# Kernel tuning notes

Measured on AMD Instinct MI355X. Metric: run time of the kernel, lower is better.

## Reference

```python
import jax, jax.numpy as jnp
import numpy as np

SCORE_THR = 0.05
IOU_THR = 0.5
MAX_PER_IMG = 100
PRE_NMS_K = 2048  # fixed candidate budget for jit-compatible NMS
NUM_CLASSES = 80
MEANS = jnp.array([0.0, 0.0, 0.0, 0.0], jnp.float32)
STDS = jnp.array([0.1, 0.1, 0.2, 0.2], jnp.float32)
WH_RATIO_CLIP = 16.0 / 1000.0


def setup_inputs() -> dict:
    key = jax.random.key(0)
    B, N, C = 4, 8192, NUM_CLASSES
    H, W = 800, 1333
    k1, k2, k3, k4, k5, k6 = jax.random.split(key, 6)
    class_outs = jax.random.normal(k1, (B * N, C + 1), jnp.float32)
    regression_outs = jax.random.normal(k2, (B * N, C * 4), jnp.float32) * 0.5
    x1 = jax.random.uniform(k3, (B, N), minval=0.0, maxval=W * 0.8)
    y1 = jax.random.uniform(k4, (B, N), minval=0.0, maxval=H * 0.8)
    w = jax.random.uniform(k5, (B, N), minval=8.0, maxval=W * 0.2)
    h = jax.random.uniform(k6, (B, N), minval=8.0, maxval=H * 0.2)
    boxes = jnp.stack([x1, y1, jnp.minimum(x1 + w, float(W)), jnp.minimum(y1 + h, float(H))], axis=-1)
    return {"class_outs": class_outs, "regression_outs": regression_outs, "boxes": boxes, "img_h": H, "img_w": W}


def delta2bbox(proposals, deltas, H, W):
    # proposals [N,4], deltas [N, C*4] -> decoded boxes [N, C, 4]
    d = deltas.reshape(deltas.shape[0], -1, 4) * STDS + MEANS
    dx, dy, dw, dh = d[..., 0], d[..., 1], d[..., 2], d[..., 3]
    max_ratio = jnp.abs(jnp.log(jnp.float32(WH_RATIO_CLIP)))
    dw = jnp.clip(dw, -max_ratio, max_ratio)
    dh = jnp.clip(dh, -max_ratio, max_ratio)
    px = (proposals[:, 0] + proposals[:, 2]) * 0.5
    py = (proposals[:, 1] + proposals[:, 3]) * 0.5
    pw = proposals[:, 2] - proposals[:, 0]
    ph = proposals[:, 3] - proposals[:, 1]
    gx = px[:, None] + pw[:, None] * dx
    gy = py[:, None] + ph[:, None] * dy
    gw = pw[:, None] * jnp.exp(dw)
    gh = ph[:, None] * jnp.exp(dh)
    x1 = jnp.clip(gx - gw * 0.5, 0.0, float(W))
    y1 = jnp.clip(gy - gh * 0.5, 0.0, float(H))
    x2 = jnp.clip(gx + gw * 0.5, 0.0, float(W))
    y2 = jnp.clip(gy + gh * 0.5, 0.0, float(H))
    return jnp.stack([x1, y1, x2, y2], axis=-1)


def pairwise_iou(b):
    # b [K,4] -> [K,K]
    area = jnp.maximum(b[:, 2] - b[:, 0], 0.0) * jnp.maximum(b[:, 3] - b[:, 1], 0.0)
    lt = jnp.maximum(b[:, None, :2], b[None, :, :2])
    rb = jnp.minimum(b[:, None, 2:], b[None, :, 2:])
    wh = jnp.clip(rb - lt, 0.0)
    inter = wh[..., 0] * wh[..., 1]
    union = area[:, None] + area[None, :] - inter
    return inter / jnp.maximum(union, 1e-6)


def per_image(cls_out, reg_out, props, H, W):
    C = NUM_CLASSES
    scores = jax.nn.softmax(cls_out, axis=-1)[:, :C]        # drop background column
    bboxes = delta2bbox(props[:, :4], reg_out, H, W)        # [N, C, 4]
    flat_s = scores.reshape(-1)                             # [N*C]
    flat_s = jnp.where(flat_s > SCORE_THR, flat_s, -1.0)
    top_s, top_i = jax.lax.top_k(flat_s, PRE_NMS_K)
    cand = bboxes.reshape(-1, 4)[top_i]                     # [K,4]
    labels = top_i % C
    valid = top_s > 0.0
    # class-aware NMS via coordinate offsets per class
    offset = labels.astype(cand.dtype)[:, None] * (float(max(H, W)) + 1.0)
    iou = pairwise_iou(cand + offset)                       # [K,K]
    idx = jnp.arange(PRE_NMS_K)

    def body(i, keep):
        sup = (iou[i] > IOU_THR) & (idx > i) & keep[i]
        return keep & ~sup

    keep = jax.lax.fori_loop(0, PRE_NMS_K, body, valid)
    fs = jnp.where(keep, top_s, -1.0)
    out_s, order = jax.lax.top_k(fs, MAX_PER_IMG)
    ok = out_s > 0.0
    det_boxes = jnp.where(ok[:, None], cand[order], 0.0)
    det_scores = jnp.where(ok, out_s, 0.0)
    det_labels = jnp.where(ok, labels[order], -1)
    det_inds = jnp.where(ok, top_i[order], -1)
    return det_boxes, det_scores, det_labels, det_inds


def reference(class_outs, regression_outs, boxes, img_h, img_w):
    B, N = boxes.shape[:2]
    cls = class_outs.reshape(B, N, -1)
    reg = regression_outs.reshape(B, N, -1)
    f = jax.vmap(lambda c, r, p: per_image(c, r, p, img_h, img_w))
    det_boxes, det_scores, det_labels, det_inds = f(cls, reg, boxes)
    return det_boxes, det_scores, det_labels, det_inds
```

## Files before the change

### kernel.cpp

```cpp
#include <hip/hip_runtime.h>
#include <cstdint>
#include <cstddef>

#pragma clang fp contract(off)

typedef unsigned long long u64;
typedef unsigned int u32;

#define B_IMG 4
#define N_ROI 8192
#define NCLS 80
#define NCOL 81
#define K_NMS 2048
#define MAXOUT 100
#define THR_SCORE 0.05f
#define THR_IOU 0.5f

#define NBIN 4096
#define BIN_OFF 62771u
#define RPI 2048
#define BLKCAP 128
#define STGN 4096

__global__ __launch_bounds__(256) void k_score(const float* __restrict__ cls,
                                               u32* __restrict__ blkcnt,
                                               u64* __restrict__ glist) {
#pragma clang fp contract(off)
  int t = threadIdx.x, wv = t >> 6, lane = t & 63;
  int wreg = blockIdx.x * 4 + wv;
  int wid0 = wreg * 4;

  const float* row0 = cls + (size_t)(wid0 + 0) * NCOL;
  const float* row1 = cls + (size_t)(wid0 + 1) * NCOL;
  const float* row2 = cls + (size_t)(wid0 + 2) * NCOL;
  const float* row3 = cls + (size_t)(wid0 + 3) * NCOL;
  float a0 = row0[lane], a1 = row1[lane], a2 = row2[lane], a3 = row3[lane];
  bool hi = lane < (NCOL - 64);
  float b0 = hi ? row0[64 + lane] : -1e38f;
  float b1 = hi ? row1[64 + lane] : -1e38f;
  float b2 = hi ? row2[64 + lane] : -1e38f;
  float b3 = hi ? row3[64 + lane] : -1e38f;

  float m0 = fmaxf(a0, b0), m1 = fmaxf(a1, b1), m2 = fmaxf(a2, b2), m3 = fmaxf(a3, b3);
#define MAXSTEP(o) \
  m0 = fmaxf(m0, __shfl_xor(m0, o)); m1 = fmaxf(m1, __shfl_xor(m1, o)); \
  m2 = fmaxf(m2, __shfl_xor(m2, o)); m3 = fmaxf(m3, __shfl_xor(m3, o));
  MAXSTEP(32) MAXSTEP(16) MAXSTEP(8) MAXSTEP(4) MAXSTEP(2) MAXSTEP(1)
#undef MAXSTEP

  float e0 = expf(a0 - m0), e1 = expf(a1 - m1), e2 = expf(a2 - m2), e3 = expf(a3 - m3);
  float f0 = hi ? expf(b0 - m0) : 0.0f;
  float f1 = hi ? expf(b1 - m1) : 0.0f;
  float f2 = hi ? expf(b2 - m2) : 0.0f;
  float f3 = hi ? expf(b3 - m3) : 0.0f;
  float s0 = e0 + f0, s1 = e1 + f1, s2 = e2 + f2, s3 = e3 + f3;
#define SUMSTEP(o) \
  s0 += __shfl_xor(s0, o); s1 += __shfl_xor(s1, o); \
  s2 += __shfl_xor(s2, o); s3 += __shfl_xor(s3, o);
  SUMSTEP(32) SUMSTEP(16) SUMSTEP(8) SUMSTEP(4) SUMSTEP(2) SUMSTEP(1)
#undef SUMSTEP

  float p0 = e0 / s0, p1 = e1 / s1, p2 = e2 / s2, p3 = e3 / s3;
  float q0 = f0 / s0, q1 = f1 / s1, q2 = f2 / s2, q3 = f3 / s3;

  u64 lm = (1ull << lane) - 1ull;
  bool lo16 = lane < 16;
  u32 base = 0;
  u64* reg = glist + (size_t)wreg * BLKCAP;

#define EMIT(R, pv, qv)                                                    \
  {                                                                        \
    bool c0 = pv > THR_SCORE;                                              \
    bool c1 = lo16 && (qv > THR_SCORE);                                    \
    u64 B0 = __ballot(c0), B1 = __ballot(c1);                              \
    int n = (wid0 + R) & (N_ROI - 1);                                      \
    if (c0) {                                                              \
      u32 pos = base + (u32)__popcll(B0 & lm);                             \
      if (pos < BLKCAP) {                                                  \
        u32 flat = (u32)(n * NCLS + lane);                                 \
        reg[pos] = ((u64)__float_as_uint(pv) << 32) | (u32)(~flat);        \
      }                                                                    \
    }                                                                      \
    if (c1) {                                                              \
      u32 pos = base + (u32)__popcll(B0) + (u32)__popcll(B1 & lm);         \
      if (pos < BLKCAP) {                                                  \
        u32 flat = (u32)(n * NCLS + 64 + lane);                            \
        reg[pos] = ((u64)__float_as_uint(qv) << 32) | (u32)(~flat);        \
      }                                                                    \
    }                                                                      \
    base += (u32)(__popcll(B0) + __popcll(B1));                            \
  }

  EMIT(0, p0, q0)
  EMIT(1, p1, q1)
  EMIT(2, p2, q2)
  EMIT(3, p3, q3)
#undef EMIT

  if (lane == 0) blkcnt[wreg] = base;
}

__global__ __launch_bounds__(1024) void k_histcut(const u32* __restrict__ blkcnt,
                                                  const u64* __restrict__ glist,
                                                  u32* __restrict__ cutg,
                                                  u32* __restrict__ binbase,
                                                  u32* __restrict__ bincnt,
                                                  u32* __restrict__ keptT) {
  __shared__ u32 lh[NBIN];
  __shared__ u32 wsum[16];
  __shared__ int best;
  __shared__ u32 cutsh;
  int b = blockIdx.x, t = threadIdx.x;
  int lane = t & 63, wv = t >> 6;

  for (int i = t; i < NBIN; i += 1024) lh[i] = 0;
  __syncthreads();

  for (int r = t; r < RPI; r += 1024) {
    u32 cnt = blkcnt[b * RPI + r];
    if (cnt > BLKCAP) cnt = BLKCAP;
    const u64* reg = glist + ((size_t)(b * RPI + r)) * BLKCAP;
    for (u32 k = 0; k < cnt; ++k) {
      u64 key = reg[k];
      atomicAdd(&lh[(u32)(key >> 46) - BIN_OFF], 1u);
    }
  }
  if (t == 0) best = 0;
  __syncthreads();

  u32 v0 = lh[t * 4 + 0], v1 = lh[t * 4 + 1], v2 = lh[t * 4 + 2], v3 = lh[t * 4 + 3];
  u32 my = v0 + v1 + v2 + v3;
  u32 inc = my;
  for (int o = 1; o < 64; o <<= 1) {
    u32 x = __shfl_up(inc, o);
    if (lane >= o) inc += x;
  }
  if (lane == 63) wsum[wv] = inc;

  u32* bc = bincnt + (size_t)b * NBIN + t * 4;
  bc[0] = 0; bc[1] = 0; bc[2] = 0; bc[3] = 0;
  __syncthreads();

  u32 wpre = 0;
  for (int i = 0; i < wv; ++i) wpre += wsum[i];
  u32 total = 0;
  for (int i = 0; i < 16; ++i) total += wsum[i];
  u32 excl = wpre + (inc - my);

  u32* bb = binbase + (size_t)b * NBIN + t * 4;
  u32 pi = excl;
  pi += v0; bb[0] = total - pi;
  pi += v1; bb[1] = total - pi;
  pi += v2; bb[2] = total - pi;
  pi += v3; bb[3] = total - pi;

  if (total >= K_NMS) {
    u32 lim = total - K_NMS;
    u32 p = excl;
    int cand = -1;
    if (p <= lim) cand = t * 4 + 0; p += v0;
    if (p <= lim) cand = t * 4 + 1; p += v1;
    if (p <= lim) cand = t * 4 + 2; p += v2;
    if (p <= lim) cand = t * 4 + 3; p += v3;
    if (cand >= 0) atomicMax(&best, cand);
  }
  __syncthreads();
  if (t == 0) {
    u32 c = (total >= K_NMS) ? (u32)best : 0u;
    cutsh = c;
    cutg[b] = c;
  }
  __syncthreads();
  u32 c = cutsh;
  if (t == (int)(c >> 2)) {
    u32 pe = excl;
    int r = (int)(c & 3);
    if (r > 0) pe += v0;
    if (r > 1) pe += v1;
    if (r > 2) pe += v2;
    keptT[b] = total - pe;
  }
}

__global__ __launch_bounds__(256) void k_scatter(const u32* __restrict__ blkcnt,
                                                 const u64* __restrict__ glist,
                                                 const u32* __restrict__ cutg,
                                                 const u32* __restrict__ binbase,
                                                 u32* __restrict__ bincnt,
                                                 u64* __restrict__ staging) {
  __shared__ u32 lcnt[32];
  __shared__ u32 mshare;
  int blk = blockIdx.x;
  int b = blk >> 6;
  int r0 = (blk & 63) * 32;
  int t = threadIdx.x;
  if (t < 32) {
    u32 cc = blkcnt[b * RPI + r0 + t];
    lcnt[t] = (cc > BLKCAP) ? BLKCAP : cc;
  }
  __syncthreads();
  if (t == 0) {
    u32 m = 0;
    for (int i = 0; i < 32; ++i) m = (lcnt[i] > m) ? lcnt[i] : m;
    mshare = m;
  }
  __syncthreads();
  u32 mmax = mshare;
  u32 cut = cutg[b];
  int r = t >> 3;
  int k0 = t & 7;
  u32 cr = lcnt[r];
  const u64* regp = glist + ((size_t)(b * RPI + r0 + r)) * BLKCAP;
  for (u32 base = 0; base < mmax; base += 8) {
    u32 k = base + k0;
    if (k < cr) {
      u64 key = regp[k];
      u32 bin = (u32)(key >> 46) - BIN_OFF;
      if (bin >= cut) {
        u32 slot = binbase[(size_t)b * NBIN + bin] +
                   atomicAdd(&bincnt[(size_t)b * NBIN + bin], 1u);
        if (slot < STGN) staging[(size_t)b * STGN + slot] = key;
      }
    }
  }
}

__global__ __launch_bounds__(256) void k_rankdecode(const u32* __restrict__ keptT,
                                                    const u32* __restrict__ binbase,
                                                    const u32* __restrict__ bincnt,
                                                    const u64* __restrict__ staging,
                                                    const float* __restrict__ props,
                                                    const float* __restrict__ regs,
                                                    const int* __restrict__ pH,
                                                    const int* __restrict__ pW,
                                                    float4* __restrict__ raw4,
                                                    float4* __restrict__ off4,
                                                    float* __restrict__ area,
                                                    float* __restrict__ scoref,
                                                    int* __restrict__ labeli,
                                                    int* __restrict__ flati) {
#pragma clang fp contract(off)
  int p0 = blockIdx.x * 256 + threadIdx.x;
  int b = p0 >> 12;
  int i = p0 & (STGN - 1);
  u32 T = keptT[b];
  if (T > STGN) T = STGN;

  if ((u32)i >= T) {
    if ((u32)i < K_NMS) {
      size_t g = (size_t)b * K_NMS + i;
      raw4[g] = make_float4(0.f, 0.f, 0.f, 0.f);
      off4[g] = make_float4(0.f, 0.f, 0.f, 0.f);
      area[g] = 0.f; scoref[g] = -1.0f; labeli[g] = 0; flati[g] = 0;
    }
    return;
  }

  u64 key = staging[(size_t)b * STGN + i];
  u32 bin = (u32)(key >> 46) - BIN_OFF;
  u32 base = binbase[(size_t)b * NBIN + bin];
  u32 cnt = bincnt[(size_t)b * NBIN + bin];
  u32 end = base + cnt;
  if (end > STGN) end = STGN;
  u32 rank = 0;
  for (u32 j = base; j < end; ++j)
    rank += (staging[(size_t)b * STGN + j] > key) ? 1u : 0u;
  u32 gslot = base + rank;
  if (gslot >= K_NMS) return;
  size_t g = (size_t)b * K_NMS + gslot;

  float Hf = (float)pH[0];
  float Wf = (float)pW[0];
  float offc = fmaxf(Hf, Wf) + 1.0f;

  u32 flat = ~(u32)(key & 0xFFFFFFFFull);
  float sc = __uint_as_float((u32)(key >> 32));
  int n = (int)(flat / NCLS);
  int c = (int)(flat - (u32)n * NCLS);

  float4 p = ((const float4*)props)[b * N_ROI + n];
  const float4 dl = *(const float4*)(regs + ((size_t)(b * N_ROI + n)) * (NCLS * 4) + c * 4);

  float mr = fabsf(logf(16.0f / 1000.0f));
  float dx = dl.x * 0.1f;
  float dy = dl.y * 0.1f;
  float dw = fminf(fmaxf(dl.z * 0.2f, -mr), mr);
  float dh = fminf(fmaxf(dl.w * 0.2f, -mr), mr);

  float px = (p.x + p.z) * 0.5f;
  float py = (p.y + p.w) * 0.5f;
  float pw = p.z - p.x;
  float ph = p.w - p.y;

  float tx = pw * dx; float gx = px + tx;
  float ty = ph * dy; float gy = py + ty;
  float gw = pw * expf(dw);
  float gh = ph * expf(dh);
  float hx = gw * 0.5f, hy = gh * 0.5f;

  float x1 = fminf(fmaxf(gx - hx, 0.0f), Wf);
  float y1 = fminf(fmaxf(gy - hy, 0.0f), Hf);
  float x2 = fminf(fmaxf(gx + hx, 0.0f), Wf);
  float y2 = fminf(fmaxf(gy + hy, 0.0f), Hf);

  raw4[g] = make_float4(x1, y1, x2, y2);

  float off = (float)c * offc;
  float ox1 = x1 + off, oy1 = y1 + off, ox2 = x2 + off, oy2 = y2 + off;
  off4[g] = make_float4(ox1, oy1, ox2, oy2);
  area[g] = fmaxf(ox2 - ox1, 0.0f) * fmaxf(oy2 - oy1, 0.0f);
  scoref[g] = sc;
  labeli[g] = c;
  flati[g] = (int)flat;
}

__global__ __launch_bounds__(256) void k_mask(const float4* __restrict__ off4,
                                              const float* __restrict__ area,
                                              u64* __restrict__ masks) {
#pragma clang fp contract(off)
  int wave = threadIdx.x >> 6, lane = threadIdx.x & 63;
  int R = blockIdx.x * 4 + wave;
  int b = R >> 11, i = R & (K_NMS - 1);
  const float4* bb = off4 + (size_t)b * K_NMS;
  const float* aa = area + (size_t)b * K_NMS;
  float4 bi = bb[i];
  float ai = aa[i];
  u64 my = 0;
  for (int w = i >> 6; w < 32; ++w) {
    int j = (w << 6) + lane;
    float4 bj = bb[j];
    float lx = fmaxf(bi.x, bj.x);
    float ly = fmaxf(bi.y, bj.y);
    float rx = fminf(bi.z, bj.z);
    float ry = fminf(bi.w, bj.w);
    float ww = fmaxf(rx - lx, 0.0f);
    float hh = fmaxf(ry - ly, 0.0f);
    float inter = ww * hh;
    float uni = (ai + aa[j]) - inter;
    float iou = inter / fmaxf(uni, 1e-6f);
    bool sup = (j > i) && (iou > THR_IOU);
    u64 word = __ballot(sup);
    if (lane == w) my = word;
  }
  if (lane < 32) masks[((size_t)R << 5) + lane] = my;
}

__global__ __launch_bounds__(64, 1) void k_scanout(const u64* __restrict__ masks,
                                                   const u32* __restrict__ keptT,
                                                   const float* __restrict__ scoref,
                                                   const float4* __restrict__ raw4,
                                                   const int* __restrict__ labeli,
                                                   const int* __restrict__ flati,
                                                   float* __restrict__ out) {
  int b = blockIdx.x;
  int lane = threadIdx.x;

  u32 Tc = keptT[b];
  if (Tc > K_NMS) Tc = K_NMS;
  u64 kw = 0;
  if (lane < 32) {
    int rem = (int)Tc - (lane << 6);
    kw = (rem >= 64) ? ~0ull : ((rem > 0) ? ((1ull << rem) - 1ull) : 0ull);
  }

  const u64* mrow = masks + ((size_t)b << 16);
  int myw = lane & 31;
  int half = lane >> 5;

  u64 dnext = mrow[((size_t)lane << 5) + 0];

  for (int c = 0; c < 32; ++c) {
    u64 dcur = dnext;
    if (c < 31) dnext = mrow[((size_t)((c + 1) * 64 + lane) << 5) + (c + 1)];

    const u64* rb = mrow + (((size_t)(c * 64 + half * 32)) << 5) + myw;
    u64 r0 = rb[0u << 5],  r1 = rb[1u << 5],  r2 = rb[2u << 5],  r3 = rb[3u << 5];
    u64 r4 = rb[4u << 5],  r5 = rb[5u << 5],  r6 = rb[6u << 5],  r7 = rb[7u << 5];
    u64 r8 = rb[8u << 5],  r9 = rb[9u << 5],  r10 = rb[10u << 5], r11 = rb[11u << 5];
    u64 r12 = rb[12u << 5], r13 = rb[13u << 5], r14 = rb[14u << 5], r15 = rb[15u << 5];
    u64 r16 = rb[16u << 5], r17 = rb[17u << 5], r18 = rb[18u << 5], r19 = rb[19u << 5];
    u64 r20 = rb[20u << 5], r21 = rb[21u << 5], r22 = rb[22u << 5], r23 = rb[23u << 5];
    u64 r24 = rb[24u << 5], r25 = rb[25u << 5], r26 = rb[26u << 5], r27 = rb[27u << 5];
    u64 r28 = rb[28u << 5], r29 = rb[29u << 5], r30 = rb[30u << 5], r31 = rb[31u << 5];
    asm volatile("" : "+v"(r0), "+v"(r1), "+v"(r2), "+v"(r3));
    asm volatile("" : "+v"(r4), "+v"(r5), "+v"(r6), "+v"(r7));
    asm volatile("" : "+v"(r8), "+v"(r9), "+v"(r10), "+v"(r11));
    asm volatile("" : "+v"(r12), "+v"(r13), "+v"(r14), "+v"(r15));
    asm volatile("" : "+v"(r16), "+v"(r17), "+v"(r18), "+v"(r19));
    asm volatile("" : "+v"(r20), "+v"(r21), "+v"(r22), "+v"(r23));
    asm volatile("" : "+v"(r24), "+v"(r25), "+v"(r26), "+v"(r27));
    asm volatile("" : "+v"(r28), "+v"(r29), "+v"(r30), "+v"(r31));

    u32 dlo = (u32)dcur, dhi = (u32)(dcur >> 32);
    u64 kc = ((u64)(u32)__builtin_amdgcn_readlane((int)(u32)(kw >> 32), c) << 32) |
             (u32)__builtin_amdgcn_readlane((int)(u32)kw, c);
#pragma unroll
    for (int d = 0; d < 64; ++d) {
      u64 dg = ((u64)(u32)__builtin_amdgcn_readlane((int)dhi, d) << 32) |
               (u32)__builtin_amdgcn_readlane((int)dlo, d);
      u64 on = (u64)0 - ((kc >> d) & 1ull);
      kc &= ~(dg & on);
    }

    u32 kb = half ? (u32)(kc >> 32) : (u32)kc;
#define ONB(r) ((u64)0 - (u64)((kb >> (r)) & 1u))
    u64 a0 = (r0 & ONB(0)) | (r1 & ONB(1)) | (r2 & ONB(2)) | (r3 & ONB(3)) |
             (r4 & ONB(4)) | (r5 & ONB(5)) | (r6 & ONB(6)) | (r7 & ONB(7));
    u64 a1 = (r8 & ONB(8)) | (r9 & ONB(9)) | (r10 & ONB(10)) | (r11 & ONB(11)) |
             (r12 & ONB(12)) | (r13 & ONB(13)) | (r14 & ONB(14)) | (r15 & ONB(15));
    u64 a2 = (r16 & ONB(16)) | (r17 & ONB(17)) | (r18 & ONB(18)) | (r19 & ONB(19)) |
             (r20 & ONB(20)) | (r21 & ONB(21)) | (r22 & ONB(22)) | (r23 & ONB(23));
    u64 a3 = (r24 & ONB(24)) | (r25 & ONB(25)) | (r26 & ONB(26)) | (r27 & ONB(27)) |
             (r28 & ONB(28)) | (r29 & ONB(29)) | (r30 & ONB(30)) | (r31 & ONB(31));
#undef ONB
    u64 supp = (a0 | a1) | (a2 | a3);
    supp |= __shfl_xor(supp, 32);
    kw &= ~supp;

    int fin = (lane <= c) ? __popcll(kw) : 0;
    for (int o = 32; o; o >>= 1) fin += __shfl_xor(fin, o);
    if (fin >= MAXOUT) break;
  }

  int pc = (lane < 32) ? __popcll(kw) : 0;
  int pre = pc;
  for (int o = 1; o < 64; o <<= 1) {
    int v = __shfl_up(pre, o);
    if (lane >= o) pre += v;
  }
  int excl = pre - pc;
  int total = __shfl(pre, 63);

  float* ob = out;
  float* os = out + B_IMG * MAXOUT * 4;
  float* ol = os + B_IMG * MAXOUT;
  float* oi = ol + B_IMG * MAXOUT;

  if (lane < 32) {
    u64 w = kw;
    int r = excl;
    while (w) {
      int bit = __ffsll((long long)w) - 1;
      w &= w - 1;
      if (r < MAXOUT) {
        int j = (lane << 6) + bit;
        size_t g = (size_t)b * K_NMS + j;
        float4 bx = raw4[g];
        int o = b * MAXOUT + r;
        ob[o * 4 + 0] = bx.x; ob[o * 4 + 1] = bx.y;
        ob[o * 4 + 2] = bx.z; ob[o * 4 + 3] = bx.w;
        os[o] = scoref[g];
        ol[o] = (float)labeli[g];
        oi[o] = (float)flati[g];
      }
      ++r;
    }
  }
  for (int r = total + lane; r < MAXOUT; r += 64) {
    int o = b * MAXOUT + r;
    ob[o * 4 + 0] = 0.f; ob[o * 4 + 1] = 0.f; ob[o * 4 + 2] = 0.f; ob[o * 4 + 3] = 0.f;
    os[o] = 0.f;
    ol[o] = -1.0f;
    oi[o] = -1.0f;
  }
}

extern "C" void kernel_launch(void* const* d_in, const int* in_sizes, int n_in,
                              void* d_out, int out_size, void* d_ws, size_t ws_size,
                              hipStream_t stream) {
  const float* cls = (const float*)d_in[0];
  const float* regs = (const float*)d_in[1];
  const float* props = (const float*)d_in[2];
  const int* pH = (const int*)d_in[3];
  const int* pW = (const int*)d_in[4];

  char* ws = (char*)d_ws;
  size_t o = 0;
  u32* blkcnt = (u32*)(ws + o); o += (size_t)B_IMG * RPI * sizeof(u32);
  u32* keptT = (u32*)(ws + o); o += 256;
  u32* cutg = (u32*)(ws + o); o += 256;
  u32* binbase = (u32*)(ws + o); o += (size_t)B_IMG * NBIN * sizeof(u32);
  u32* bincnt = (u32*)(ws + o); o += (size_t)B_IMG * NBIN * sizeof(u32);
  u64* glist = (u64*)(ws + o); o += (size_t)B_IMG * RPI * BLKCAP * sizeof(u64);
  u64* staging = (u64*)(ws + o); o += (size_t)B_IMG * STGN * sizeof(u64);
  float4* raw4 = (float4*)(ws + o); o += (size_t)B_IMG * K_NMS * sizeof(float4);
  float4* off4 = (float4*)(ws + o); o += (size_t)B_IMG * K_NMS * sizeof(float4);
  float* area = (float*)(ws + o); o += (size_t)B_IMG * K_NMS * sizeof(float);
  float* scoref = (float*)(ws + o); o += (size_t)B_IMG * K_NMS * sizeof(float);
  int* labeli = (int*)(ws + o); o += (size_t)B_IMG * K_NMS * sizeof(int);
  int* flati = (int*)(ws + o); o += (size_t)B_IMG * K_NMS * sizeof(int);
  u64* masks = (u64*)(ws + o); o += (size_t)B_IMG * K_NMS * 32 * sizeof(u64);

  k_score<<<B_IMG * RPI / 4, 256, 0, stream>>>(cls, blkcnt, glist);
  k_histcut<<<B_IMG, 1024, 0, stream>>>(blkcnt, glist, cutg, binbase, bincnt, keptT);
  k_scatter<<<256, 256, 0, stream>>>(blkcnt, glist, cutg, binbase, bincnt, staging);
  k_rankdecode<<<B_IMG * STGN / 256, 256, 0, stream>>>(keptT, binbase, bincnt, staging,
                                                       props, regs, pH, pW,
                                                       raw4, off4, area, scoref, labeli, flati);
  k_mask<<<B_IMG * K_NMS / 4, 256, 0, stream>>>(off4, area, masks);
  k_scanout<<<B_IMG, 64, 0, stream>>>(masks, keptT, scoref, raw4, labeli, flati, (float*)d_out);
}
```

Before: 67.26 us.

## Fuse histogram and scatter per image, stage NMS boxes in LDS for mask

Merges the histogram/cutoff kernel with the scatter kernel so each image's single 1024-thread block scatters candidates using shared-memory bin bases and counters instead of global atomics. This removes one launch and the global bincnt zeroing and atomic traffic. The cost is that the scatter is no longer spread over 256 blocks, so it runs on only 4 blocks. The IoU mask kernel now loads all 2048 boxes and areas for an image into LDS and has each wave process four rows, which cuts repeated global loads at the price of fewer, larger blocks.

```diff
diff --git a/kernel.cpp b/kernel.cpp
--- a/kernel.cpp
+++ b/kernel.cpp
@@ -100,13 +100,14 @@
   if (lane == 0) blkcnt[wreg] = base;
 }
 
-__global__ __launch_bounds__(1024) void k_histcut(const u32* __restrict__ blkcnt,
-                                                  const u64* __restrict__ glist,
-                                                  u32* __restrict__ cutg,
-                                                  u32* __restrict__ binbase,
-                                                  u32* __restrict__ bincnt,
-                                                  u32* __restrict__ keptT) {
+__global__ __launch_bounds__(1024) void k_histscat(const u32* __restrict__ blkcnt,
+                                                   const u64* __restrict__ glist,
+                                                   u32* __restrict__ binbase_g,
+                                                   u32* __restrict__ bincnt_g,
+                                                   u32* __restrict__ keptT,
+                                                   u64* __restrict__ staging) {
   __shared__ u32 lh[NBIN];
+  __shared__ u32 lbb[NBIN];
   __shared__ u32 wsum[16];
   __shared__ int best;
   __shared__ u32 cutsh;
@@ -136,9 +137,6 @@
     if (lane >= o) inc += x;
   }
   if (lane == 63) wsum[wv] = inc;
-
-  u32* bc = bincnt + (size_t)b * NBIN + t * 4;
-  bc[0] = 0; bc[1] = 0; bc[2] = 0; bc[3] = 0;
   __syncthreads();
 
   u32 wpre = 0;
@@ -147,12 +145,16 @@
   for (int i = 0; i < 16; ++i) total += wsum[i];
   u32 excl = wpre + (inc - my);
 
-  u32* bb = binbase + (size_t)b * NBIN + t * 4;
+  u32 bb0, bb1, bb2, bb3;
   u32 pi = excl;
-  pi += v0; bb[0] = total - pi;
-  pi += v1; bb[1] = total - pi;
-  pi += v2; bb[2] = total - pi;
-  pi += v3; bb[3] = total - pi;
+  pi += v0; bb0 = total - pi;
+  pi += v1; bb1 = total - pi;
+  pi += v2; bb2 = total - pi;
+  pi += v3; bb3 = total - pi;
+  lbb[t * 4 + 0] = bb0; lbb[t * 4 + 1] = bb1;
+  lbb[t * 4 + 2] = bb2; lbb[t * 4 + 3] = bb3;
+  u32* gb = binbase_g + (size_t)b * NBIN + t * 4;
+  gb[0] = bb0; gb[1] = bb1; gb[2] = bb2; gb[3] = bb3;
 
   if (total >= K_NMS) {
     u32 lim = total - K_NMS;
@@ -165,64 +167,40 @@
     if (cand >= 0) atomicMax(&best, cand);
   }
   __syncthreads();
-  if (t == 0) {
-    u32 c = (total >= K_NMS) ? (u32)best : 0u;
-    cutsh = c;
-    cutg[b] = c;
-  }
-  __syncthreads();
-  u32 c = cutsh;
-  if (t == (int)(c >> 2)) {
+  if (t == 0) cutsh = (total >= K_NMS) ? (u32)best : 0u;
+  __syncthreads();
+  u32 cut = cutsh;
+  if (t == (int)(cut >> 2)) {
     u32 pe = excl;
-    int r = (int)(c & 3);
+    int r = (int)(cut & 3);
     if (r > 0) pe += v0;
     if (r > 1) pe += v1;
     if (r > 2) pe += v2;
     keptT[b] = total - pe;
   }
-}
-
-__global__ __launch_bounds__(256) void k_scatter(const u32* __restrict__ blkcnt,
-                                                 const u64* __restrict__ glist,
-                                                 const u32* __restrict__ cutg,
-                                                 const u32* __restrict__ binbase,
-                                                 u32* __restrict__ bincnt,
-                                                 u64* __restrict__ staging) {
-  __shared__ u32 lcnt[32];
-  __shared__ u32 mshare;
-  int blk = blockIdx.x;
-  int b = blk >> 6;
-  int r0 = (blk & 63) * 32;
-  int t = threadIdx.x;
-  if (t < 32) {
-    u32 cc = blkcnt[b * RPI + r0 + t];
-    lcnt[t] = (cc > BLKCAP) ? BLKCAP : cc;
-  }
-  __syncthreads();
-  if (t == 0) {
-    u32 m = 0;
-    for (int i = 0; i < 32; ++i) m = (lcnt[i] > m) ? lcnt[i] : m;
-    mshare = m;
-  }
-  __syncthreads();
-  u32 mmax = mshare;
-  u32 cut = cutg[b];
-  int r = t >> 3;
-  int k0 = t & 7;
-  u32 cr = lcnt[r];
-  const u64* regp = glist + ((size_t)(b * RPI + r0 + r)) * BLKCAP;
-  for (u32 base = 0; base < mmax; base += 8) {
-    u32 k = base + k0;
-    if (k < cr) {
-      u64 key = regp[k];
+
+  lh[t * 4 + 0] = 0; lh[t * 4 + 1] = 0; lh[t * 4 + 2] = 0; lh[t * 4 + 3] = 0;
+  __syncthreads();
+
+  u64* stg = staging + (size_t)b * STGN;
+  for (int r = t; r < RPI; r += 1024) {
+    u32 cnt = blkcnt[b * RPI + r];
+    if (cnt > BLKCAP) cnt = BLKCAP;
+    const u64* reg = glist + ((size_t)(b * RPI + r)) * BLKCAP;
+    for (u32 k = 0; k < cnt; ++k) {
+      u64 key = reg[k];
       u32 bin = (u32)(key >> 46) - BIN_OFF;
       if (bin >= cut) {
-        u32 slot = binbase[(size_t)b * NBIN + bin] +
-                   atomicAdd(&bincnt[(size_t)b * NBIN + bin], 1u);
-        if (slot < STGN) staging[(size_t)b * STGN + slot] = key;
+        u32 slot = lbb[bin] + atomicAdd(&lh[bin], 1u);
+        if (slot < STGN) stg[slot] = key;
       }
     }
   }
+  __syncthreads();
+
+  u32* gc = bincnt_g + (size_t)b * NBIN + t * 4;
+  gc[0] = lh[t * 4 + 0]; gc[1] = lh[t * 4 + 1];
+  gc[2] = lh[t * 4 + 2]; gc[3] = lh[t * 4 + 3];
 }
 
 __global__ __launch_bounds__(256) void k_rankdecode(const u32* __restrict__ keptT,
@@ -318,31 +296,41 @@
                                               const float* __restrict__ area,
                                               u64* __restrict__ masks) {
 #pragma clang fp contract(off)
-  int wave = threadIdx.x >> 6, lane = threadIdx.x & 63;
-  int R = blockIdx.x * 4 + wave;
-  int b = R >> 11, i = R & (K_NMS - 1);
+  __shared__ float4 sb[K_NMS];
+  __shared__ float sa[K_NMS];
+  int blk = blockIdx.x;
+  int b = blk >> 7;
+  int r0 = (blk & 127) << 4;
+  int t = threadIdx.x;
   const float4* bb = off4 + (size_t)b * K_NMS;
   const float* aa = area + (size_t)b * K_NMS;
-  float4 bi = bb[i];
-  float ai = aa[i];
-  u64 my = 0;
-  for (int w = i >> 6; w < 32; ++w) {
-    int j = (w << 6) + lane;
-    float4 bj = bb[j];
-    float lx = fmaxf(bi.x, bj.x);
-    float ly = fmaxf(bi.y, bj.y);
-    float rx = fminf(bi.z, bj.z);
-    float ry = fminf(bi.w, bj.w);
-    float ww = fmaxf(rx - lx, 0.0f);
-    float hh = fmaxf(ry - ly, 0.0f);
-    float inter = ww * hh;
-    float uni = (ai + aa[j]) - inter;
-    float iou = inter / fmaxf(uni, 1e-6f);
-    bool sup = (j > i) && (iou > THR_IOU);
-    u64 word = __ballot(sup);
-    if (lane == w) my = word;
-  }
-  if (lane < 32) masks[((size_t)R << 5) + lane] = my;
+  for (int i = t; i < K_NMS; i += 256) { sb[i] = bb[i]; sa[i] = aa[i]; }
+  __syncthreads();
+
+  int wave = t >> 6, lane = t & 63;
+  for (int rr = 0; rr < 4; ++rr) {
+    int i = r0 + (wave << 2) + rr;
+    float4 bi = sb[i];
+    float ai = sa[i];
+    u64 my = 0;
+    for (int w = i >> 6; w < 32; ++w) {
+      int j = (w << 6) + lane;
+      float4 bj = sb[j];
+      float lx = fmaxf(bi.x, bj.x);
+      float ly = fmaxf(bi.y, bj.y);
+      float rx = fminf(bi.z, bj.z);
+      float ry = fminf(bi.w, bj.w);
+      float ww = fmaxf(rx - lx, 0.0f);
+      float hh = fmaxf(ry - ly, 0.0f);
+      float inter = ww * hh;
+      float uni = (ai + sa[j]) - inter;
+      float iou = inter / fmaxf(uni, 1e-6f);
+      bool sup = (j > i) && (iou > THR_IOU);
+      u64 word = __ballot(sup);
+      if (lane == w) my = word;
+    }
+    if (lane < 32) masks[((size_t)(b * K_NMS + i) << 5) + lane] = my;
+  }
 }
 
 __global__ __launch_bounds__(64, 1) void k_scanout(const u64* __restrict__ masks,
@@ -478,7 +466,6 @@
   size_t o = 0;
   u32* blkcnt = (u32*)(ws + o); o += (size_t)B_IMG * RPI * sizeof(u32);
   u32* keptT = (u32*)(ws + o); o += 256;
-  u32* cutg = (u32*)(ws + o); o += 256;
   u32* binbase = (u32*)(ws + o); o += (size_t)B_IMG * NBIN * sizeof(u32);
   u32* bincnt = (u32*)(ws + o); o += (size_t)B_IMG * NBIN * sizeof(u32);
   u64* glist = (u64*)(ws + o); o += (size_t)B_IMG * RPI * BLKCAP * sizeof(u64);
@@ -492,11 +479,10 @@
   u64* masks = (u64*)(ws + o); o += (size_t)B_IMG * K_NMS * 32 * sizeof(u64);
 
   k_score<<<B_IMG * RPI / 4, 256, 0, stream>>>(cls, blkcnt, glist);
-  k_histcut<<<B_IMG, 1024, 0, stream>>>(blkcnt, glist, cutg, binbase, bincnt, keptT);
-  k_scatter<<<256, 256, 0, stream>>>(blkcnt, glist, cutg, binbase, bincnt, staging);
+  k_histscat<<<B_IMG, 1024, 0, stream>>>(blkcnt, glist, binbase, bincnt, keptT, staging);
   k_rankdecode<<<B_IMG * STGN / 256, 256, 0, stream>>>(keptT, binbase, bincnt, staging,
                                                        props, regs, pH, pW,
                                                        raw4, off4, area, scoref, labeli, flati);
-  k_mask<<<B_IMG * K_NMS / 4, 256, 0, stream>>>(off4, area, masks);
+  k_mask<<<B_IMG * 128, 256, 0, stream>>>(off4, area, masks);
   k_scanout<<<B_IMG, 64, 0, stream>>>(masks, keptT, scoref, raw4, labeli, flati, (float*)d_out);
 }
```

Result: slower. 83.09 us (+23.5%).
